# Kernel tuning notes

Hardware: AMD Instinct MI355X
Metric: run time of the kernel (lower is better)

The kernel has to match this reference:

```python
import jax, jax.numpy as jnp
import numpy as np

B = 256; N1 = 10240; E1 = 81920; N3 = 25600; E3 = 819200; D = 128


def _seg_softmax(logits, seg, n):
    m = jax.ops.segment_max(logits, seg, num_segments=n)
    e = jnp.exp(logits - m[seg])
    s = jax.ops.segment_sum(e, seg, num_segments=n)
    return e / s[seg]


def _gat(x, src, dst, W, a_src, a_dst, bias, n):
    # PyG GATConv, heads=1, add_self_loops (src/dst already include self loops)
    h = x @ W
    logit = jax.nn.leaky_relu(h[src] @ a_src + h[dst] @ a_dst, 0.2)
    alpha = _seg_softmax(logit, dst, n)
    return jax.ops.segment_sum(h[src] * alpha[:, None], dst, num_segments=n) + bias


def _gcn(x, row, col, w, W, bias, n):
    # PyG GCNConv with edge_weight, self loops already appended with weight 1
    deg = jax.ops.segment_sum(w, col, num_segments=n)
    dinv = jnp.where(deg > 0, jax.lax.rsqrt(jnp.maximum(deg, 1e-12)), 0.0)
    norm = dinv[row] * w * dinv[col]
    return jax.ops.segment_sum((x @ W)[row] * norm[:, None], col, num_segments=n) + bias


def _mean_pool(x, batch, nb):
    s = jax.ops.segment_sum(x, batch, num_segments=nb)
    cnt = jax.ops.segment_sum(jnp.ones((x.shape[0],), x.dtype), batch, num_segments=nb)
    return s / jnp.maximum(cnt, 1.0)[:, None]


def _bn(x, g, b, m, v, eps=1e-5):
    # eval-mode BatchNorm1d (running stats)
    return (x - m) * jax.lax.rsqrt(v + eps) * g + b


def _forward(x1, x3, ami_dis, ami_dis_li, fc00_w, fc00_b, fc01_w, fc01_b, fc02_w, fc02_b, w1, b1, w2, b2, fc03_w, fc03_b, gat_W, gat_as, gat_ad, gat_bias, vn_emb, vl1_w, vl1_b, bn1_g, bn1_b, bn1_m, bn1_v, vl2_w, vl2_b, bn2_g, bn2_b, bn2_m, bn2_v, gcn_W, gcn_b, fc1_w, fc1_b, fc2_w, fc2_b, fc3_w, fc3_b, out_w, out_b, drug_ei, ami_ei, batch1, ami_batch):
    relu = jax.nn.relu
    a = relu(x3 @ fc00_w + fc00_b)
    a = relu(a @ fc01_w + fc01_b)
    a = relu(a @ fc02_w + fc02_b)
    a = jnp.concatenate([a, ami_dis_li[:, None]], axis=1)  # [N3,128]
    sl3 = jnp.arange(N3)
    row = jnp.concatenate([ami_ei[0], sl3])
    col = jnp.concatenate([ami_ei[1], sl3])
    ew = jnp.concatenate([ami_dis, jnp.ones((N3,), a.dtype)])
    a = relu(_gcn(a, row, col, ew, gcn_W[0], gcn_b[0], N3)); p1 = _mean_pool(a, ami_batch, B)
    a = relu(_gcn(a, row, col, ew, gcn_W[1], gcn_b[1], N3)); p2 = _mean_pool(a, ami_batch, B)
    a = relu(_gcn(a, row, col, ew, gcn_W[2], gcn_b[2], N3)); p3 = _mean_pool(a, ami_batch, B)
    ami = p1 + p2 + p3
    h = relu(x1 @ w1 + b1)
    h = relu(h @ w2 + b2)
    h = h @ fc03_w + fc03_b
    vx = jnp.broadcast_to(vn_emb[None, :], (B, D))  # vn_emb(zeros) = row0 for every graph
    x = h + 0.2 * vx[batch1]
    sl1 = jnp.arange(N1)
    src = jnp.concatenate([drug_ei[0], sl1])
    dst = jnp.concatenate([drug_ei[1], sl1])
    x11 = relu(_gat(x, src, dst, gat_W[0], gat_as[0], gat_ad[0], gat_bias[0], N1))
    # virtual-node update (linear is Identity since in==out; eval mode: dropout off, residual False)
    t = jax.ops.segment_sum(x11, batch1, num_segments=B) + vx
    t = relu(_bn(t @ vl1_w + vl1_b, bn1_g, bn1_b, bn1_m, bn1_v))
    drug = relu(_bn(t @ vl2_w + vl2_b, bn2_g, bn2_b, bn2_m, bn2_v))
    x = x11 + 0.2 * drug[batch1]
    x12 = relu(_gat(x, src, dst, gat_W[1], gat_as[1], gat_ad[1], gat_bias[1], N1))
    x13 = relu(_gat(x, src, dst, gat_W[2], gat_as[2], gat_ad[2], gat_bias[2], N1))
    xg = _mean_pool(x11 + x12 + x13, batch1, B)
    # --- fused head ---
    z = jnp.concatenate([xg, ami], axis=1)  # [B,256]
    h2 = z @ fc1_w + fc1_b
    z = relu(h2)
    z = relu(z @ fc2_w + fc2_b)
    z = relu(z @ fc3_w + fc3_b)
    out = z @ out_w + out_b
    return out, h2


def setup_inputs() -> dict:
    key = jax.random.key(0)
    ks = iter(jax.random.split(key, 80))
    def nrm(*s):
        return jax.random.normal(next(ks), s, jnp.float32) * 0.05
    inp = {}
    inp['x1'] = jax.random.normal(next(ks), (N1, 52), jnp.float32)
    inp['x3'] = jax.random.normal(next(ks), (N3, 1900), jnp.float32)
    inp['ami_dis'] = jax.random.uniform(next(ks), (E3,), jnp.float32) + 0.1
    inp['ami_dis_li'] = jax.random.normal(next(ks), (N3,), jnp.float32)
    inp['fc00_w'] = nrm(1900, 1024); inp['fc00_b'] = nrm(1024)
    inp['fc01_w'] = nrm(1024, 512); inp['fc01_b'] = nrm(512)
    inp['fc02_w'] = nrm(512, 127); inp['fc02_b'] = nrm(127)
    inp['w1'] = nrm(52, 128); inp['b1'] = nrm(128)
    inp['w2'] = nrm(128, 64); inp['b2'] = nrm(64)
    inp['fc03_w'] = nrm(64, 128); inp['fc03_b'] = nrm(128)
    inp['gat_W'] = nrm(3, 128, 128); inp['gat_as'] = nrm(3, 128)
    inp['gat_ad'] = nrm(3, 128); inp['gat_bias'] = nrm(3, 128)
    inp['vn_emb'] = jnp.zeros((128,), jnp.float32)
    inp['vl1_w'] = nrm(128, 256); inp['vl1_b'] = nrm(256)
    inp['bn1_g'] = jnp.ones((256,), jnp.float32); inp['bn1_b'] = jnp.zeros((256,), jnp.float32)
    inp['bn1_m'] = jnp.zeros((256,), jnp.float32); inp['bn1_v'] = jnp.ones((256,), jnp.float32)
    inp['vl2_w'] = nrm(256, 128); inp['vl2_b'] = nrm(128)
    inp['bn2_g'] = jnp.ones((128,), jnp.float32); inp['bn2_b'] = jnp.zeros((128,), jnp.float32)
    inp['bn2_m'] = jnp.zeros((128,), jnp.float32); inp['bn2_v'] = jnp.ones((128,), jnp.float32)
    inp['gcn_W'] = nrm(3, 128, 128); inp['gcn_b'] = nrm(3, 128)
    inp['fc1_w'] = nrm(256, 512); inp['fc1_b'] = nrm(512)
    inp['fc2_w'] = nrm(512, 256); inp['fc2_b'] = nrm(256)
    inp['fc3_w'] = nrm(256, 128); inp['fc3_b'] = nrm(128)
    inp['out_w'] = nrm(128, 1); inp['out_b'] = nrm(1)
    inp['drug_ei'] = jax.random.randint(next(ks), (2, E1), 0, N1)
    inp['ami_ei'] = jax.random.randint(next(ks), (2, E3), 0, N3)
    inp['batch1'] = jnp.repeat(jnp.arange(B), N1 // B)
    inp['ami_batch'] = jnp.repeat(jnp.arange(B), N3 // B)
    return inp


def reference(x1, x3, ami_dis, ami_dis_li, fc00_w, fc00_b, fc01_w, fc01_b, fc02_w, fc02_b, w1, b1, w2, b2, fc03_w, fc03_b, gat_W, gat_as, gat_ad, gat_bias, vn_emb, vl1_w, vl1_b, bn1_g, bn1_b, bn1_m, bn1_v, vl2_w, vl2_b, bn2_g, bn2_b, bn2_m, bn2_v, gcn_W, gcn_b, fc1_w, fc1_b, fc2_w, fc2_b, fc3_w, fc3_b, out_w, out_b, drug_ei, ami_ei, batch1, ami_batch):
    return _forward(x1, x3, ami_dis, ami_dis_li, fc00_w, fc00_b, fc01_w, fc01_b, fc02_w, fc02_b, w1, b1, w2, b2, fc03_w, fc03_b, gat_W, gat_as, gat_ad, gat_bias, vn_emb, vl1_w, vl1_b, bn1_g, bn1_b, bn1_m, bn1_v, vl2_w, vl2_b, bn2_g, bn2_b, bn2_m, bn2_v, gcn_W, gcn_b, fc1_w, fc1_b, fc2_w, fc2_b, fc3_w, fc3_b, out_w, out_b, drug_ei, ami_ei, batch1, ami_batch)
```

## Files before the change

### kernel.cpp

```cpp
#include <hip/hip_runtime.h>
#include <hip/hip_bf16.h>
#include <stdint.h>

typedef __hip_bfloat16 bf16;
typedef __attribute__((ext_vector_type(8))) short short8;
typedef __attribute__((ext_vector_type(4))) float f32x4;

#define BB 256
#define NN1 10240
#define EE1 81920
#define NN3 25600
#define EE3 819200

__device__ __forceinline__ void load16_g2l(const void* g, void* l) {
  __builtin_amdgcn_global_load_lds(
      (const __attribute__((address_space(1))) void*)(uintptr_t)g,
      (__attribute__((address_space(3))) void*)(uintptr_t)l, 16, 0, 0);
}

__device__ __forceinline__ unsigned short f2bfbits(float v) {
  bf16 t = __float2bfloat16(v);
  union { bf16 b; unsigned short u; } x; x.b = t; return x.u;
}

// ... 4 lines not shown
  if (i >= M * nch) return;
  int r = i / nch, c8 = (i - r * nch) << 3;
  const float* s = in + (size_t)r * K + c8;
  short8 o;
  if (c8 + 8 <= K) {
    float4 a = *(const float4*)s, b = *(const float4*)(s + 4);
    o[0] = f2bfbits(a.x); o[1] = f2bfbits(a.y); o[2] = f2bfbits(a.z); o[3] = f2bfbits(a.w);
    o[4] = f2bfbits(b.x); o[5] = f2bfbits(b.y); o[6] = f2bfbits(b.z); o[7] = f2bfbits(b.w);
  } else {
#pragma unroll
    for (int j = 0; j < 8; j++) o[j] = f2bfbits(c8 + j < K ? s[j] : 0.f);
  }
  *(short8*)&out[(size_t)r * Kp + c8] = o;
}

__global__ void cast8(const float* __restrict__ in, bf16* __restrict__ out, int n8) {
  int i = blockIdx.x * blockDim.x + threadIdx.x;
  if (i >= n8) return;
  const float* s = in + (size_t)i * 8;
  float4 a = *(const float4*)s, b = *(const float4*)(s + 4);
  short8 o;
  o[0] = f2bfbits(a.x); o[1] = f2bfbits(a.y); o[2] = f2bfbits(a.z); o[3] = f2bfbits(a.w);
  o[4] = f2bfbits(b.x); o[5] = f2bfbits(b.y); o[6] = f2bfbits(b.z); o[7] = f2bfbits(b.w);
  *(short8*)&out[(size_t)i * 8] = o;
}

__global__ void transpose_cast_bf(const float* __restrict__ in, bf16* __restrict__ out,
                                  int K, int N, int Kp, int Np) {
  __shared__ float tile[32][33];
  int k0 = blockIdx.x * 32, n0 = blockIdx.y * 32;
  int tx = threadIdx.x, ty = threadIdx.y;
#pragma unroll
  for (int j = 0; j < 32; j += 8) {
    int k = k0 + ty + j, n = n0 + tx;
    tile[ty + j][tx] = (k < K && n < N) ? in[(size_t)k * N + n] : 0.f;
  }
  __syncthreads();
#pragma unroll
  for (int j = 0; j < 32; j += 8) {
    int n = n0 + ty + j, k = k0 + tx;
    if (n < Np && k < Kp) out[(size_t)n * Kp + k] = __float2bfloat16(tile[tx][ty + j]);
  }
}

template<int RELU, int OUT_F32, int CONCAT_LI>
__global__ __launch_bounds__(256) void gemm_mfma(
    const bf16* __restrict__ A, const bf16* __restrict__ Bt,
    const float* __restrict__ bias, void* __restrict__ Cout,
    const float* __restrict__ li, int M, int N, int K)
{
  __shared__ __align__(16) unsigned short sA[128 * 32];
  __shared__ __align__(16) unsigned short sB[128 * 32];
  const int nBN = N >> 7;
  const int bm = blockIdx.x / nBN, bn = blockIdx.x - bm * nBN;
  const size_t m0 = (size_t)bm << 7, n0 = (size_t)bn << 7;
  const int t = threadIdx.x;
  const int lane = t & 63, wave = t >> 6;
  const int wr = wave >> 1, wc = wave & 1;
  const int srow = t >> 2;
  const int scol = (t & 3) << 3;
  const bf16* Ab = A + (m0 + srow) * (size_t)K + scol;
  const bf16* Bb = Bt + (n0 + srow) * (size_t)K + scol;
  unsigned short* sAd = &sA[srow * 32 + scol];
  unsigned short* sBd = &sB[srow * 32 + scol];
  const int lr = lane & 15;
  const int lk = (lane >> 4) << 3;

  f32x4 zero = {0.f, 0.f, 0.f, 0.f};
  f32x4 acc[4][4];
// ... 13 lines not shown
    for (int i = 0; i < 4; i++) af[i] = *(const short8*)&sA[(wr * 64 + i * 16 + lr) * 32 + lk];
#pragma unroll
    for (int i = 0; i < 4; i++) bv[i] = *(const short8*)&sB[(wc * 64 + i * 16 + lr) * 32 + lk];
#pragma unroll
    for (int i = 0; i < 4; i++)
#pragma unroll
      for (int j = 0; j < 4; j++)
        acc[i][j] = __builtin_amdgcn_mfma_f32_16x16x32_bf16(af[i], bv[j], acc[i][j], 0, 0, 0);
    __syncthreads();
  }

  const int crow = wr * 64, ccol = wc * 64;
#pragma unroll
  for (int i = 0; i < 4; i++) {
#pragma unroll
    for (int j = 0; j < 4; j++) {
      const size_t gc = n0 + ccol + j * 16 + lr;
      const bool isLi = CONCAT_LI && (gc == (size_t)(N - 1));
      float bvf = (!isLi && bias) ? bias[gc] : 0.f;
#pragma unroll
      for (int v = 0; v < 4; v++) {
        const size_t gr = m0 + crow + i * 16 + (lane >> 4) * 4 + v;
        float val = acc[i][j][v] + bvf;
        if (RELU) val = fmaxf(val, 0.f);
        if (isLi) val = li[gr];
        if (OUT_F32) ((float*)Cout)[gr * N + gc] = val;
        else ((bf16*)Cout)[gr * N + gc] = __float2bfloat16(val);
      }
    }
  }
}

template<int RELU, int BN>
__global__ void gemm_simt(const float* __restrict__ A, const float* __restrict__ W,
                          const float* __restrict__ bias, const float* __restrict__ vnadd,
                          const float* __restrict__ bng, const float* __restrict__ bnb,
                          const float* __restrict__ bnm, const float* __restrict__ bnv,
                          float* __restrict__ C, int M, int N, int K)
{
  int idx = blockIdx.x * blockDim.x + threadIdx.x;
  if (idx >= M * N) return;
  int m = idx / N, n = idx - m * N;
  const float* a = A + (size_t)m * K;
  float acc = bias[n];
  if (vnadd) acc += 0.2f * vnadd[n];
  for (int k = 0; k < K; k++) acc = fmaf(a[k], W[(size_t)k * N + n], acc);
  if (BN) acc = (acc - bnm[n]) * rsqrtf(bnv[n] + 1e-5f) * bng[n] + bnb[n];
  if (RELU) acc = fmaxf(acc, 0.f);
  C[idx] = acc;
}

__global__ void hist_csr(const int* __restrict__ dstA, int E, int Etot, int* __restrict__ cnt) {
  int e = blockIdx.x * blockDim.x + threadIdx.x;
  if (e >= Etot) return;
  int t = (e < E) ? dstA[e] : e - E;
  atomicAdd(&cnt[t], 1);
}

__global__ void exscan(const int* __restrict__ cnt, int* __restrict__ base, int n) {
  const int tid = threadIdx.x, lane = tid & 63, wid = tid >> 6;
  __shared__ int wsum[16];
  __shared__ int woff[17];
  __shared__ int carry;
  if (tid == 0) carry = 0;
  __syncthreads();
  for (int off = 0; off < n; off += 1024) {
    int i = off + tid;
    int v = (i < n) ? cnt[i] : 0;
    int iv = v;
#pragma unroll
    for (int s = 1; s < 64; s <<= 1) {
      int tt = __shfl_up(iv, s);
      if (lane >= s) iv += tt;
    }
    if (lane == 63) wsum[wid] = iv;
    __syncthreads();
    if (tid == 0) {
      int run = 0;
      for (int j = 0; j < 16; j++) { woff[j] = run; run += wsum[j]; }
      woff[16] = run;
    }
    __syncthreads();
    if (i < n) base[i] = carry + woff[wid] + iv - v;
    __syncthreads();
    if (tid == 0) carry += woff[16];
    __syncthreads();
  }
  if (threadIdx.x == 0) base[n] = carry;
}

__global__ void fill_csr(const int* __restrict__ srcA, const int* __restrict__ dstA,
                         const float* __restrict__ w, const float* __restrict__ dinv,
                         const int* __restrict__ base, int* __restrict__ cur,
                         int2* __restrict__ rec, int E, int Etot) {
  int e = blockIdx.x * blockDim.x + threadIdx.x;
  if (e >= Etot) return;
  int s, t; float ww = 1.f;
  if (e < E) { s = srcA[e]; t = dstA[e]; if (w) ww = w[e]; }
  else { s = t = e - E; }
  int pos = base[t] + atomicAdd(&cur[t], 1);
  float nrm = dinv ? (dinv[s] * ww * dinv[t]) : 0.f;
  rec[pos] = make_int2(s, __float_as_int(nrm));
}

__global__ void deg_kernel(const int* __restrict__ col, const float* __restrict__ w,
                           float* __restrict__ deg, int E) {
  int e = blockIdx.x * blockDim.x + threadIdx.x;
  if (e < E) atomicAdd(&deg[col[e]], w[e]);
}

__global__ void dinv_kernel(const float* __restrict__ deg, float* __restrict__ dinv, int n) {
  int i = blockIdx.x * blockDim.x + threadIdx.x;
  if (i >= n) return;
  float d = deg[i] + 1.0f;
  dinv[i] = d > 0.f ? rsqrtf(fmaxf(d, 1e-12f)) : 0.f;
}

__global__ void gcn_gather(const int* __restrict__ base, const int2* __restrict__ rec,
                           const float* __restrict__ h, const float* __restrict__ bias,
                           bf16* __restrict__ aout, float* __restrict__ pool,
                           const int* __restrict__ batch, int n) {
  int wid = threadIdx.x >> 6, lane = threadIdx.x & 63;
  int node = blockIdx.x * 4 + wid;
  if (node >= n) return;
  int s0 = base[node], s1 = base[node + 1];
  float2 acc = {0.f, 0.f};
  for (int p = s0; p < s1; p++) {
    int2 r = rec[p];
    float nrm = __int_as_float(r.y);
    float2 hv = *(const float2*)&h[(size_t)r.x * 128 + lane * 2];
    acc.x += hv.x * nrm; acc.y += hv.y * nrm;
  }
  int d0 = lane * 2;
  float v0 = fmaxf(acc.x + bias[d0], 0.f);
  float v1 = fmaxf(acc.y + bias[d0 + 1], 0.f);
  __hip_bfloat162 pr; pr.x = __float2bfloat16(v0); pr.y = __float2bfloat16(v1);
  *(__hip_bfloat162*)&aout[(size_t)node * 128 + d0] = pr;
  int g = batch[node];
  atomicAdd(&pool[(size_t)g * 128 + d0], v0);
  atomicAdd(&pool[(size_t)g * 128 + d0 + 1], v1);
}

__global__ void gat_uv(const float* __restrict__ h, const float* __restrict__ as,
                       const float* __restrict__ ad, float* __restrict__ u,
                       float* __restrict__ v, int n) {
  int wave = threadIdx.x >> 6, lane = threadIdx.x & 63;
  int row = blockIdx.x * 4 + wave;
  if (row >= n) return;
  const float* hr = h + (size_t)row * 128;
  float su = 0.f, sv = 0.f;
  for (int d = lane; d < 128; d += 64) { float x = hr[d]; su += x * as[d]; sv += x * ad[d]; }
  for (int off = 32; off; off >>= 1) { su += __shfl_down(su, off); sv += __shfl_down(sv, off); }
  if (lane == 0) { u[row] = su; v[row] = sv; }
}

__global__ void gat_gather(const int* __restrict__ base, const int2* __restrict__ rec,
                           const float* __restrict__ u, const float* __restrict__ vv,
                           const float* __restrict__ h, const float* __restrict__ bias,
                           float* __restrict__ xout, float* __restrict__ pool,
                           const int* __restrict__ batch, int n) {
  int wid = threadIdx.x >> 6, lane = threadIdx.x & 63;
  int node = blockIdx.x * 4 + wid;
  if (node >= n) return;
  int s0 = base[node], s1 = base[node + 1];
  float vt = vv[node];
  float m = -3.4e38f;
  for (int p = s0 + lane; p < s1; p += 64) {
    float lg = u[rec[p].x] + vt; lg = lg >= 0.f ? lg : 0.2f * lg;
    m = fmaxf(m, lg);
  }
#pragma unroll
  for (int s = 32; s; s >>= 1) m = fmaxf(m, __shfl_xor(m, s));
  float ssum = 0.f;
  for (int p = s0 + lane; p < s1; p += 64) {
    float lg = u[rec[p].x] + vt; lg = lg >= 0.f ? lg : 0.2f * lg;
    ssum += __expf(lg - m);
  }
#pragma unroll
  for (int s = 32; s; s >>= 1) ssum += __shfl_xor(ssum, s);
  float rs = 1.f / ssum;
  float2 acc = {0.f, 0.f};
  for (int p = s0; p < s1; p++) {
    int2 r = rec[p];
    float lg = u[r.x] + vt; lg = lg >= 0.f ? lg : 0.2f * lg;
    float alpha = __expf(lg - m) * rs;
    float2 hv = *(const float2*)&h[(size_t)r.x * 128 + lane * 2];
    acc.x += hv.x * alpha; acc.y += hv.y * alpha;
  }
  int d0 = lane * 2;
  float v0 = fmaxf(acc.x + bias[d0], 0.f);
  float v1 = fmaxf(acc.y + bias[d0 + 1], 0.f);
  if (xout) *(float2*)&xout[(size_t)node * 128 + d0] = make_float2(v0, v1);
  int g = batch[node];
  atomicAdd(&pool[(size_t)g * 128 + d0], v0);
  atomicAdd(&pool[(size_t)g * 128 + d0 + 1], v1);
}

__global__ void cnt_kernel(const int* __restrict__ batch, float* __restrict__ cnt, int n) {
  int i = blockIdx.x * blockDim.x + threadIdx.x;
  if (i < n) atomicAdd(&cnt[batch[i]], 1.0f);
}

__global__ void pool_div(const float* __restrict__ pool, const float* __restrict__ cnt,
                         float* __restrict__ out, int n) {
  int i = blockIdx.x * blockDim.x + threadIdx.x;
  if (i < n) out[i] = pool[i] / fmaxf(cnt[i >> 7], 1.f);
}

__global__ void fill_t(float* __restrict__ t, const float* __restrict__ vn, int n) {
  int i = blockIdx.x * blockDim.x + threadIdx.x;
  if (i < n) t[i] = vn[i & 127];
}

__global__ void scatter_t(const float* __restrict__ x, const int* __restrict__ batch,
                          float* __restrict__ t, int n) {
  int gi = blockIdx.x * blockDim.x + threadIdx.x;
  if (gi >= n) return;
  int i = gi >> 7, d = gi & 127;
  atomicAdd(&t[(size_t)batch[i] * 128 + d], x[gi]);
}

__global__ void add_drug(const float* __restrict__ x11, const float* __restrict__ dr,
                         const int* __restrict__ batch, float* __restrict__ out, int n) {
  int gi = blockIdx.x * blockDim.x + threadIdx.x;
  if (gi >= n) return;
  int i = gi >> 7, d = gi & 127;
  out[gi] = x11[gi] + 0.2f * dr[(size_t)batch[i] * 128 + d];
}

__global__ void concat_k(const float* __restrict__ xg, const float* __restrict__ ami,
                         float* __restrict__ z, int n) {
  int i = blockIdx.x * blockDim.x + threadIdx.x;
  if (i >= n) return;
  int b = i >> 8, d = i & 255;
  z[i] = d < 128 ? xg[(b << 7) + d] : ami[(b << 7) + d - 128];
}

__global__ void relu_k(const float* __restrict__ in, float* __restrict__ out, int n) {
  int i = blockIdx.x * blockDim.x + threadIdx.x;
  if (i < n) out[i] = fmaxf(in[i], 0.f);
}

static inline int cdiv(int a, int b) { return (a + b - 1) / b; }

extern "C" void kernel_launch(void* const* d_in, const int* in_sizes, int n_in,
                              void* d_out, int out_size, void* d_ws, size_t ws_size,
                              hipStream_t stream)
{
  const float* x1      = (const float*)d_in[0];
  const float* x3      = (const float*)d_in[1];
  const float* ami_dis = (const float*)d_in[2];
  const float* ami_li  = (const float*)d_in[3];
  const float* fc00_w = (const float*)d_in[4];  const float* fc00_b = (const float*)d_in[5];
  const float* fc01_w = (const float*)d_in[6];  const float* fc01_b = (const float*)d_in[7];
  const float* fc02_w = (const float*)d_in[8];  const float* fc02_b = (const float*)d_in[9];
// ... 19 lines not shown
  const int* batch1    = (const int*)d_in[45];
  const int* ami_batch = (const int*)d_in[46];

  char* ws = (char*)d_ws;
  bf16*  Bt0   = (bf16*)(ws + 0);
  bf16*  Bt1   = (bf16*)(ws + 3932160);
  bf16*  Bt2   = (bf16*)(ws + 4980736);
  bf16*  BtGCN = (bf16*)(ws + 5111808);
  bf16*  BtGAT = (bf16*)(ws + 5210112);
  float* deg   = (float*)(ws + 5308416);
  float* dinv  = (float*)(ws + 5410816);
  float* pool_ami  = (float*)(ws + 5513216);
  float* pool_drug = (float*)(ws + 5644288);
  float* cnt_ami   = (float*)(ws + 5775360);
  float* cnt_drug  = (float*)(ws + 5776384);
  float* amivec    = (float*)(ws + 5777408);
  float* xg        = (float*)(ws + 5908480);
  float* uarr  = (float*)(ws + 6039552);
  float* varr  = (float*)(ws + 6080512);
  float* tbuf  = (float*)(ws + 6572032);
  float* t2buf = (float*)(ws + 6703104);
  float* drugv = (float*)(ws + 6965248);
  float* zbuf  = (float*)(ws + 7096320);
  float* z2buf = (float*)(ws + 7358464);
  float* z3buf = (float*)(ws + 7882752);
  float* z4buf = (float*)(ws + 8144896);

  const size_t AA = 8388608;
  bf16*  A3bf = (bf16*)(ws + AA);
  bf16*  a2bf = (bf16*)(ws + AA);
  bf16*  abf  = (bf16*)(ws + AA + 41943040);
  float* hG   = (float*)(ws + AA + 52428800);
  int*  base3 = (int*) (ws + AA + 68157440);
  int*  cur3  = (int*) (ws + AA + 68812800);
  int2* rec3  = (int2*)(ws + AA + 69206016);
  int*  base1 = (int*) (ws + AA + 77594624);
  int*  cur1  = (int*) (ws + AA + 78118912);
  int2* rec1  = (int2*)(ws + AA + 78643200);
  float* h1    = (float*)(ws + AA + 0);
  float* hd2   = (float*)(ws + AA + 5242880);
  float* xdrug = (float*)(ws + AA + 7864320);
  float* x11   = (float*)(ws + AA + 13107200);
  float* x2b   = (float*)(ws + AA + 18350080);
  bf16*  xbf   = (bf16*) (ws + AA + 23592960);
  bf16*  xbf2  = (bf16*) (ws + AA + 26214400);
  float* hgat  = (float*)(ws + AA + 28835840);
  const size_t ABo = AA + 98304000;
  bf16*  a1bf = (bf16*)(ws + ABo);

  const int Etot3 = EE3 + NN3, Etot1 = EE1 + NN1;

  {
    dim3 b(32, 8);
    transpose_cast_bf<<<dim3(60, 32), b, 0, stream>>>(fc00_w, Bt0, 1900, 1024, 1920, 1024);
    transpose_cast_bf<<<dim3(32, 16), b, 0, stream>>>(fc01_w, Bt1, 1024, 512, 1024, 512);
    transpose_cast_bf<<<dim3(16, 4), b, 0, stream>>>(fc02_w, Bt2, 512, 127, 512, 128);
    for (int l = 0; l < 3; l++) {
      transpose_cast_bf<<<dim3(4, 4), b, 0, stream>>>(gcn_W + l * 16384, BtGCN + l * 16384, 128, 128, 128, 128);
      transpose_cast_bf<<<dim3(4, 4), b, 0, stream>>>(gat_W + l * 16384, BtGAT + l * 16384, 128, 128, 128, 128);
    }
  }
  cast_pad8<<<cdiv(25600 * 240, 256), 256, 0, stream>>>(x3, A3bf, 25600, 1900, 1920);

  gemm_mfma<1, 0, 0><<<200 * 8, 256, 0, stream>>>(A3bf, Bt0, fc00_b, a1bf, nullptr, 25600, 1024, 1920);
  gemm_mfma<1, 0, 0><<<200 * 4, 256, 0, stream>>>(a1bf, Bt1, fc01_b, a2bf, nullptr, 25600, 512, 1024);
  gemm_mfma<1, 0, 1><<<200 * 1, 256, 0, stream>>>(a2bf, Bt2, fc02_b, abf, ami_li, 25600, 128, 512);

  hipMemsetAsync(deg, 0, 102400, stream);
  hipMemsetAsync(pool_ami, 0, 131072, stream);
  hipMemsetAsync(pool_drug, 0, 131072, stream);
  hipMemsetAsync(cnt_ami, 0, 1024, stream);
  hipMemsetAsync(cnt_drug, 0, 1024, stream);
  deg_kernel<<<cdiv(EE3, 256), 256, 0, stream>>>(ami_ei + EE3, ami_dis, deg, EE3);
  dinv_kernel<<<cdiv(NN3, 256), 256, 0, stream>>>(deg, dinv, NN3);
  cnt_kernel<<<cdiv(NN3, 256), 256, 0, stream>>>(ami_batch, cnt_ami, NN3);
  cnt_kernel<<<cdiv(NN1, 256), 256, 0, stream>>>(batch1, cnt_drug, NN1);

  hipMemsetAsync(cur3, 0, 102400, stream);
  hist_csr<<<cdiv(Etot3, 256), 256, 0, stream>>>(ami_ei + EE3, EE3, Etot3, cur3);
  exscan<<<1, 1024, 0, stream>>>(cur3, base3, NN3);
  hipMemsetAsync(cur3, 0, 102400, stream);
  fill_csr<<<cdiv(Etot3, 256), 256, 0, stream>>>(ami_ei, ami_ei + EE3, ami_dis, dinv,
                                                 base3, cur3, rec3, EE3, Etot3);
  hipMemsetAsync(cur1, 0, 40960, stream);
  hist_csr<<<cdiv(Etot1, 256), 256, 0, stream>>>(drug_ei + EE1, EE1, Etot1, cur1);
  exscan<<<1, 1024, 0, stream>>>(cur1, base1, NN1);
  hipMemsetAsync(cur1, 0, 40960, stream);
  fill_csr<<<cdiv(Etot1, 256), 256, 0, stream>>>(drug_ei, drug_ei + EE1, nullptr, nullptr,
                                                 base1, cur1, rec1, EE1, Etot1);

  for (int l = 0; l < 3; l++) {
    gemm_mfma<0, 1, 0><<<200, 256, 0, stream>>>(abf, BtGCN + l * 16384, nullptr, hG, nullptr, NN3, 128, 128);
    gcn_gather<<<cdiv(NN3, 4), 256, 0, stream>>>(base3, rec3, hG, gcn_b + l * 128,
                                                 abf, pool_ami, ami_batch, NN3);
  }
  pool_div<<<cdiv(BB * 128, 256), 256, 0, stream>>>(pool_ami, cnt_ami, amivec, BB * 128);

  gemm_simt<1, 0><<<cdiv(NN1 * 128, 256), 256, 0, stream>>>(x1, w1, b1, nullptr, nullptr, nullptr, nullptr, nullptr, h1, NN1, 128, 52);
  gemm_simt<1, 0><<<cdiv(NN1 * 64, 256), 256, 0, stream>>>(h1, w2, b2, nullptr, nullptr, nullptr, nullptr, nullptr, hd2, NN1, 64, 128);
  gemm_simt<0, 0><<<cdiv(NN1 * 128, 256), 256, 0, stream>>>(hd2, fc03_w, fc03_b, vn_emb, nullptr, nullptr, nullptr, nullptr, xdrug, NN1, 128, 64);
  cast8<<<cdiv(NN1 * 16, 256), 256, 0, stream>>>(xdrug, xbf, NN1 * 16);

  gemm_mfma<0, 1, 0><<<80, 256, 0, stream>>>(xbf, BtGAT, nullptr, hgat, nullptr, NN1, 128, 128);
  gat_uv<<<cdiv(NN1, 4), 256, 0, stream>>>(hgat, gat_as, gat_ad, uarr, varr, NN1);
  gat_gather<<<cdiv(NN1, 4), 256, 0, stream>>>(base1, rec1, uarr, varr, hgat, gat_bias,
                                               x11, pool_drug, batch1, NN1);

  fill_t<<<cdiv(BB * 128, 256), 256, 0, stream>>>(tbuf, vn_emb, BB * 128);
  scatter_t<<<cdiv(NN1 * 128, 256), 256, 0, stream>>>(x11, batch1, tbuf, NN1 * 128);
  gemm_simt<1, 1><<<cdiv(BB * 256, 256), 256, 0, stream>>>(tbuf, vl1_w, vl1_b, nullptr, bn1_g, bn1_b, bn1_m, bn1_v, t2buf, BB, 256, 128);
  gemm_simt<1, 1><<<cdiv(BB * 128, 256), 256, 0, stream>>>(t2buf, vl2_w, vl2_b, nullptr, bn2_g, bn2_b, bn2_m, bn2_v, drugv, BB, 128, 256);
  add_drug<<<cdiv(NN1 * 128, 256), 256, 0, stream>>>(x11, drugv, batch1, x2b, NN1 * 128);
  cast8<<<cdiv(NN1 * 16, 256), 256, 0, stream>>>(x2b, xbf2, NN1 * 16);

  for (int l = 1; l < 3; l++) {
    gemm_mfma<0, 1, 0><<<80, 256, 0, stream>>>(xbf2, BtGAT + l * 16384, nullptr, hgat, nullptr, NN1, 128, 128);
    gat_uv<<<cdiv(NN1, 4), 256, 0, stream>>>(hgat, gat_as + l * 128, gat_ad + l * 128, uarr, varr, NN1);
    gat_gather<<<cdiv(NN1, 4), 256, 0, stream>>>(base1, rec1, uarr, varr, hgat, gat_bias + l * 128,
                                                 nullptr, pool_drug, batch1, NN1);
  }
  pool_div<<<cdiv(BB * 128, 256), 256, 0, stream>>>(pool_drug, cnt_drug, xg, BB * 128);

  concat_k<<<cdiv(BB * 256, 256), 256, 0, stream>>>(xg, amivec, zbuf, BB * 256);
  float* h2out = (float*)d_out + 256;
  gemm_simt<0, 0><<<cdiv(BB * 512, 256), 256, 0, stream>>>(zbuf, fc1_w, fc1_b, nullptr, nullptr, nullptr, nullptr, nullptr, h2out, BB, 512, 256);
  relu_k<<<cdiv(BB * 512, 256), 256, 0, stream>>>(h2out, z2buf, BB * 512);
  gemm_simt<1, 0><<<cdiv(BB * 256, 256), 256, 0, stream>>>(z2buf, fc2_w, fc2_b, nullptr, nullptr, nullptr, nullptr, nullptr, z3buf, BB, 256, 512);
  gemm_simt<1, 0><<<cdiv(BB * 128, 256), 256, 0, stream>>>(z3buf, fc3_w, fc3_b, nullptr, nullptr, nullptr, nullptr, nullptr, z4buf, BB, 128, 256);
  gemm_simt<0, 0><<<1, 256, 0, stream>>>(z4buf, out_w, out_b, nullptr, nullptr, nullptr, nullptr, nullptr, (float*)d_out, BB, 1, 128);
}
```

Measured before the change: 2.030 ms.

## Reorder GCN to aggregate-then-transform, fuse drug MLP and head, bf16 GAT features

The GCN layers now aggregate bf16 node features first and then run the MFMA GEMM, with bias, ReLU and mean-pool atomics fused into its epilogue. The drug MLP becomes one per-node fused kernel, and the classifier head is fused into a single kernel. GAT hidden states are stored in bf16, and the single-block CSR scan is replaced by a three-kernel multi-block scan. Small kernels and memsets are merged and the GEMM grid gets a block swizzle. These changes cut launches, memory traffic and the serial scan, at the cost of extra bf16 rounding on intermediates and per-element pooling atomics in the GEMM epilogue.

```diff
diff --git a/kernel.cpp b/kernel.cpp
--- a/kernel.cpp
+++ b/kernel.cpp
@@ -42,20 +42,11 @@
   *(short8*)&out[(size_t)r * Kp + c8] = o;
 }
 
-__global__ void cast8(const float* __restrict__ in, bf16* __restrict__ out, int n8) {
-  int i = blockIdx.x * blockDim.x + threadIdx.x;
-  if (i >= n8) return;
-  const float* s = in + (size_t)i * 8;
-  float4 a = *(const float4*)s, b = *(const float4*)(s + 4);
-  short8 o;
-  o[0] = f2bfbits(a.x); o[1] = f2bfbits(a.y); o[2] = f2bfbits(a.z); o[3] = f2bfbits(a.w);
-  o[4] = f2bfbits(b.x); o[5] = f2bfbits(b.y); o[6] = f2bfbits(b.z); o[7] = f2bfbits(b.w);
-  *(short8*)&out[(size_t)i * 8] = o;
-}
-
 __global__ void transpose_cast_bf(const float* __restrict__ in, bf16* __restrict__ out,
                                   int K, int N, int Kp, int Np) {
   __shared__ float tile[32][33];
+  in  += (size_t)blockIdx.z * K * N;
+  out += (size_t)blockIdx.z * Kp * Np;
   int k0 = blockIdx.x * 32, n0 = blockIdx.y * 32;
   int tx = threadIdx.x, ty = threadIdx.y;
 #pragma unroll
@@ -71,16 +62,19 @@
   }
 }
 
-template<int RELU, int OUT_F32, int CONCAT_LI>
+template<int RELU, int OUT_F32, int CONCAT_LI, int POOL>
 __global__ __launch_bounds__(256) void gemm_mfma(
     const bf16* __restrict__ A, const bf16* __restrict__ Bt,
     const float* __restrict__ bias, void* __restrict__ Cout,
-    const float* __restrict__ li, int M, int N, int K)
+    const float* __restrict__ li, float* __restrict__ pool,
+    const int* __restrict__ batch, int M, int N, int K)
 {
   __shared__ __align__(16) unsigned short sA[128 * 32];
   __shared__ __align__(16) unsigned short sB[128 * 32];
   const int nBN = N >> 7;
-  const int bm = blockIdx.x / nBN, bn = blockIdx.x - bm * nBN;
+  int bid = blockIdx.x, nwg = gridDim.x;
+  int swz = (nwg & 7) ? bid : ((bid & 7) * (nwg >> 3) + (bid >> 3));
+  const int bm = swz / nBN, bn = swz - bm * nBN;
   const size_t m0 = (size_t)bm << 7, n0 = (size_t)bn << 7;
   const int t = threadIdx.x;
   const int lane = t & 63, wave = t >> 6;
@@ -124,18 +118,20 @@
 #pragma unroll
   for (int i = 0; i < 4; i++) {
 #pragma unroll
-    for (int j = 0; j < 4; j++) {
-      const size_t gc = n0 + ccol + j * 16 + lr;
-      const bool isLi = CONCAT_LI && (gc == (size_t)(N - 1));
-      float bvf = (!isLi && bias) ? bias[gc] : 0.f;
-#pragma unroll
-      for (int v = 0; v < 4; v++) {
-        const size_t gr = m0 + crow + i * 16 + (lane >> 4) * 4 + v;
-        float val = acc[i][j][v] + bvf;
+    for (int v = 0; v < 4; v++) {
+      const size_t gr = m0 + crow + i * 16 + (lane >> 4) * 4 + v;
+      const int bt = POOL ? batch[gr] : 0;
+      const float liv = CONCAT_LI ? li[gr] : 0.f;
+#pragma unroll
+      for (int j = 0; j < 4; j++) {
+        const size_t gc = n0 + ccol + j * 16 + lr;
+        const bool isLi = CONCAT_LI && (gc == (size_t)(N - 1));
+        float val = acc[i][j][v] + ((!isLi && bias) ? bias[gc] : 0.f);
         if (RELU) val = fmaxf(val, 0.f);
-        if (isLi) val = li[gr];
+        if (isLi) val = liv;
         if (OUT_F32) ((float*)Cout)[gr * N + gc] = val;
         else ((bf16*)Cout)[gr * N + gc] = __float2bfloat16(val);
+        if (POOL) atomicAdd(&pool[(size_t)bt * 128 + gc], val);
       }
     }
   }
@@ -143,7 +139,7 @@
 
 template<int RELU, int BN>
 __global__ void gemm_simt(const float* __restrict__ A, const float* __restrict__ W,
-                          const float* __restrict__ bias, const float* __restrict__ vnadd,
+                          const float* __restrict__ bias,
                           const float* __restrict__ bng, const float* __restrict__ bnb,
                           const float* __restrict__ bnm, const float* __restrict__ bnv,
                           float* __restrict__ C, int M, int N, int K)
@@ -153,7 +149,6 @@
   int m = idx / N, n = idx - m * N;
   const float* a = A + (size_t)m * K;
   float acc = bias[n];
-  if (vnadd) acc += 0.2f * vnadd[n];
   for (int k = 0; k < K; k++) acc = fmaf(a[k], W[(size_t)k * N + n], acc);
   if (BN) acc = (acc - bnm[n]) * rsqrtf(bnv[n] + 1e-5f) * bng[n] + bnb[n];
   if (RELU) acc = fmaxf(acc, 0.f);
@@ -167,36 +162,36 @@
   atomicAdd(&cnt[t], 1);
 }
 
-__global__ void exscan(const int* __restrict__ cnt, int* __restrict__ base, int n) {
+__global__ void scan_blocks(const int* __restrict__ cnt, int* __restrict__ base,
+                            int* __restrict__ bsum, int n) {
   const int tid = threadIdx.x, lane = tid & 63, wid = tid >> 6;
-  __shared__ int wsum[16];
-  __shared__ int woff[17];
-  __shared__ int carry;
-  if (tid == 0) carry = 0;
-  __syncthreads();
-  for (int off = 0; off < n; off += 1024) {
-    int i = off + tid;
-    int v = (i < n) ? cnt[i] : 0;
-    int iv = v;
-#pragma unroll
-    for (int s = 1; s < 64; s <<= 1) {
-      int tt = __shfl_up(iv, s);
-      if (lane >= s) iv += tt;
-    }
-    if (lane == 63) wsum[wid] = iv;
-    __syncthreads();
-    if (tid == 0) {
-      int run = 0;
-      for (int j = 0; j < 16; j++) { woff[j] = run; run += wsum[j]; }
-      woff[16] = run;
-    }
-    __syncthreads();
-    if (i < n) base[i] = carry + woff[wid] + iv - v;
-    __syncthreads();
-    if (tid == 0) carry += woff[16];
-    __syncthreads();
-  }
-  if (threadIdx.x == 0) base[n] = carry;
+  __shared__ int wsum[16], woff[16];
+  __shared__ int tot;
+  int i = blockIdx.x * 1024 + tid;
+  int v = (i < n) ? cnt[i] : 0;
+  int iv = v;
+#pragma unroll
+  for (int s = 1; s < 64; s <<= 1) { int t = __shfl_up(iv, s); if (lane >= s) iv += t; }
+  if (lane == 63) wsum[wid] = iv;
+  __syncthreads();
+  if (tid == 0) { int run = 0; for (int j = 0; j < 16; j++) { woff[j] = run; run += wsum[j]; } tot = run; }
+  __syncthreads();
+  if (i < n) base[i] = woff[wid] + iv - v;
+  if (tid == 0) bsum[blockIdx.x] = tot;
+}
+
+__global__ void scan_tops(int* __restrict__ bsum, int* __restrict__ base, int n, int nb) {
+  if (threadIdx.x == 0) {
+    int run = 0;
+    for (int j = 0; j < nb; j++) { int t = bsum[j]; bsum[j] = run; run += t; }
+    base[n] = run;
+  }
+}
+
+__global__ void scan_add(int* __restrict__ base, const int* __restrict__ bsum,
+                         int* __restrict__ cur, int n) {
+  int i = blockIdx.x * 1024 + threadIdx.x;
+  if (i < n) { base[i] += bsum[blockIdx.x]; cur[i] = 0; }
 }
 
 __global__ void fill_csr(const int* __restrict__ srcA, const int* __restrict__ dstA,
@@ -226,47 +221,44 @@
   dinv[i] = d > 0.f ? rsqrtf(fmaxf(d, 1e-12f)) : 0.f;
 }
 
-__global__ void gcn_gather(const int* __restrict__ base, const int2* __restrict__ rec,
-                           const float* __restrict__ h, const float* __restrict__ bias,
-                           bf16* __restrict__ aout, float* __restrict__ pool,
-                           const int* __restrict__ batch, int n) {
+__global__ void gather_pre(const int* __restrict__ base, const int2* __restrict__ rec,
+                           const bf16* __restrict__ x, bf16* __restrict__ y, int n) {
   int wid = threadIdx.x >> 6, lane = threadIdx.x & 63;
   int node = blockIdx.x * 4 + wid;
   if (node >= n) return;
   int s0 = base[node], s1 = base[node + 1];
-  float2 acc = {0.f, 0.f};
+  int d0 = lane * 2;
+  float a0 = 0.f, a1 = 0.f;
   for (int p = s0; p < s1; p++) {
     int2 r = rec[p];
     float nrm = __int_as_float(r.y);
-    float2 hv = *(const float2*)&h[(size_t)r.x * 128 + lane * 2];
-    acc.x += hv.x * nrm; acc.y += hv.y * nrm;
-  }
-  int d0 = lane * 2;
-  float v0 = fmaxf(acc.x + bias[d0], 0.f);
-  float v1 = fmaxf(acc.y + bias[d0 + 1], 0.f);
-  __hip_bfloat162 pr; pr.x = __float2bfloat16(v0); pr.y = __float2bfloat16(v1);
-  *(__hip_bfloat162*)&aout[(size_t)node * 128 + d0] = pr;
-  int g = batch[node];
-  atomicAdd(&pool[(size_t)g * 128 + d0], v0);
-  atomicAdd(&pool[(size_t)g * 128 + d0 + 1], v1);
-}
-
-__global__ void gat_uv(const float* __restrict__ h, const float* __restrict__ as,
+    __hip_bfloat162 hv = *(const __hip_bfloat162*)&x[(size_t)r.x * 128 + d0];
+    a0 = fmaf(__bfloat162float(hv.x), nrm, a0);
+    a1 = fmaf(__bfloat162float(hv.y), nrm, a1);
+  }
+  __hip_bfloat162 pr; pr.x = __float2bfloat16(a0); pr.y = __float2bfloat16(a1);
+  *(__hip_bfloat162*)&y[(size_t)node * 128 + d0] = pr;
+}
+
+__global__ void gat_uv(const bf16* __restrict__ h, const float* __restrict__ as,
                        const float* __restrict__ ad, float* __restrict__ u,
                        float* __restrict__ v, int n) {
   int wave = threadIdx.x >> 6, lane = threadIdx.x & 63;
   int row = blockIdx.x * 4 + wave;
   if (row >= n) return;
-  const float* hr = h + (size_t)row * 128;
-  float su = 0.f, sv = 0.f;
-  for (int d = lane; d < 128; d += 64) { float x = hr[d]; su += x * as[d]; sv += x * ad[d]; }
+  int d0 = lane * 2;
+  __hip_bfloat162 hv = *(const __hip_bfloat162*)&h[(size_t)row * 128 + d0];
+  float x0 = __bfloat162float(hv.x), x1 = __bfloat162float(hv.y);
+  float su = x0 * as[d0] + x1 * as[d0 + 1];
+  float sv = x0 * ad[d0] + x1 * ad[d0 + 1];
+#pragma unroll
   for (int off = 32; off; off >>= 1) { su += __shfl_down(su, off); sv += __shfl_down(sv, off); }
   if (lane == 0) { u[row] = su; v[row] = sv; }
 }
 
 __global__ void gat_gather(const int* __restrict__ base, const int2* __restrict__ rec,
                            const float* __restrict__ u, const float* __restrict__ vv,
-                           const float* __restrict__ h, const float* __restrict__ bias,
+                           const bf16* __restrict__ h, const float* __restrict__ bias,
                            float* __restrict__ xout, float* __restrict__ pool,
                            const int* __restrict__ batch, int n) {
   int wid = threadIdx.x >> 6, lane = threadIdx.x & 63;
@@ -289,66 +281,125 @@
 #pragma unroll
   for (int s = 32; s; s >>= 1) ssum += __shfl_xor(ssum, s);
   float rs = 1.f / ssum;
-  float2 acc = {0.f, 0.f};
+  int d0 = lane * 2;
+  float a0 = 0.f, a1 = 0.f;
   for (int p = s0; p < s1; p++) {
     int2 r = rec[p];
     float lg = u[r.x] + vt; lg = lg >= 0.f ? lg : 0.2f * lg;
     float alpha = __expf(lg - m) * rs;
-    float2 hv = *(const float2*)&h[(size_t)r.x * 128 + lane * 2];
-    acc.x += hv.x * alpha; acc.y += hv.y * alpha;
-  }
-  int d0 = lane * 2;
-  float v0 = fmaxf(acc.x + bias[d0], 0.f);
-  float v1 = fmaxf(acc.y + bias[d0 + 1], 0.f);
+    __hip_bfloat162 hv = *(const __hip_bfloat162*)&h[(size_t)r.x * 128 + d0];
+    a0 = fmaf(__bfloat162float(hv.x), alpha, a0);
+    a1 = fmaf(__bfloat162float(hv.y), alpha, a1);
+  }
+  float v0 = fmaxf(a0 + bias[d0], 0.f);
+  float v1 = fmaxf(a1 + bias[d0 + 1], 0.f);
   if (xout) *(float2*)&xout[(size_t)node * 128 + d0] = make_float2(v0, v1);
   int g = batch[node];
   atomicAdd(&pool[(size_t)g * 128 + d0], v0);
   atomicAdd(&pool[(size_t)g * 128 + d0 + 1], v1);
 }
 
+__global__ void mlp_drug(const float* __restrict__ x1, const float* __restrict__ w1,
+                         const float* __restrict__ b1, const float* __restrict__ w2,
+                         const float* __restrict__ b2, const float* __restrict__ w3,
+                         const float* __restrict__ b3, const float* __restrict__ vn,
+                         bf16* __restrict__ xout, int n) {
+  __shared__ float l1[4][128];
+  __shared__ float l2[4][64];
+  int wid = threadIdx.x >> 6, lane = threadIdx.x & 63;
+  int node = blockIdx.x * 4 + wid;
+  const float* xr = x1 + (size_t)node * 52;
+  int d0 = lane * 2;
+  float a0 = b1[d0], a1 = b1[d0 + 1];
+  for (int k = 0; k < 52; k++) {
+    float xk = xr[k];
+    a0 = fmaf(xk, w1[k * 128 + d0], a0); a1 = fmaf(xk, w1[k * 128 + d0 + 1], a1);
+  }
+  l1[wid][d0] = fmaxf(a0, 0.f); l1[wid][d0 + 1] = fmaxf(a1, 0.f);
+  __syncthreads();
+  float h2 = b2[lane];
+  for (int k = 0; k < 128; k++) h2 = fmaf(l1[wid][k], w2[k * 64 + lane], h2);
+  l2[wid][lane] = fmaxf(h2, 0.f);
+  __syncthreads();
+  float o0 = b3[d0] + 0.2f * vn[d0], o1 = b3[d0 + 1] + 0.2f * vn[d0 + 1];
+  for (int k = 0; k < 64; k++) {
+    float hk = l2[wid][k];
+    o0 = fmaf(hk, w3[k * 128 + d0], o0); o1 = fmaf(hk, w3[k * 128 + d0 + 1], o1);
+  }
+  __hip_bfloat162 pr; pr.x = __float2bfloat16(o0); pr.y = __float2bfloat16(o1);
+  *(__hip_bfloat162*)&xout[(size_t)node * 128 + d0] = pr;
+}
+
 __global__ void cnt_kernel(const int* __restrict__ batch, float* __restrict__ cnt, int n) {
   int i = blockIdx.x * blockDim.x + threadIdx.x;
   if (i < n) atomicAdd(&cnt[batch[i]], 1.0f);
 }
 
-__global__ void pool_div(const float* __restrict__ pool, const float* __restrict__ cnt,
-                         float* __restrict__ out, int n) {
+__global__ void tvn_k(const float* __restrict__ pool, const float* __restrict__ vn,
+                      float* __restrict__ t, int n) {
   int i = blockIdx.x * blockDim.x + threadIdx.x;
-  if (i < n) out[i] = pool[i] / fmaxf(cnt[i >> 7], 1.f);
-}
-
-__global__ void fill_t(float* __restrict__ t, const float* __restrict__ vn, int n) {
+  if (i < n) t[i] = pool[i] + vn[i & 127];
+}
+
+__global__ void add_cast(const float* __restrict__ x11, const float* __restrict__ dr,
+                         const int* __restrict__ batch, bf16* __restrict__ out, int n2) {
   int i = blockIdx.x * blockDim.x + threadIdx.x;
-  if (i < n) t[i] = vn[i & 127];
-}
-
-__global__ void scatter_t(const float* __restrict__ x, const int* __restrict__ batch,
-                          float* __restrict__ t, int n) {
-  int gi = blockIdx.x * blockDim.x + threadIdx.x;
-  if (gi >= n) return;
-  int i = gi >> 7, d = gi & 127;
-  atomicAdd(&t[(size_t)batch[i] * 128 + d], x[gi]);
-}
-
-__global__ void add_drug(const float* __restrict__ x11, const float* __restrict__ dr,
-                         const int* __restrict__ batch, float* __restrict__ out, int n) {
-  int gi = blockIdx.x * blockDim.x + threadIdx.x;
-  if (gi >= n) return;
-  int i = gi >> 7, d = gi & 127;
-  out[gi] = x11[gi] + 0.2f * dr[(size_t)batch[i] * 128 + d];
-}
-
-__global__ void concat_k(const float* __restrict__ xg, const float* __restrict__ ami,
-                         float* __restrict__ z, int n) {
-  int i = blockIdx.x * blockDim.x + threadIdx.x;
-  if (i >= n) return;
-  int b = i >> 8, d = i & 255;
-  z[i] = d < 128 ? xg[(b << 7) + d] : ami[(b << 7) + d - 128];
-}
-
-__global__ void relu_k(const float* __restrict__ in, float* __restrict__ out, int n) {
-  int i = blockIdx.x * blockDim.x + threadIdx.x;
-  if (i < n) out[i] = fmaxf(in[i], 0.f);
+  if (i >= n2) return;
+  int node = i >> 6, d0 = (i & 63) << 1;
+  const float* drb = dr + (size_t)batch[node] * 128 + d0;
+  float2 xv = *(const float2*)&x11[(size_t)node * 128 + d0];
+  __hip_bfloat162 pr;
+  pr.x = __float2bfloat16(xv.x + 0.2f * drb[0]);
+  pr.y = __float2bfloat16(xv.y + 0.2f * drb[1]);
+  *(__hip_bfloat162*)&out[(size_t)node * 128 + d0] = pr;
+}
+
+__global__ __launch_bounds__(256) void head_fused(
+    const float* __restrict__ pool_d, const float* __restrict__ cnt_d,
+    const float* __restrict__ pool_a, const float* __restrict__ cnt_a,
+    const float* __restrict__ fc1_w, const float* __restrict__ fc1_b,
+    const float* __restrict__ fc2_w, const float* __restrict__ fc2_b,
+    const float* __restrict__ fc3_w, const float* __restrict__ fc3_b,
+    const float* __restrict__ ow, const float* __restrict__ ob,
+    float* __restrict__ out, float* __restrict__ h2out) {
+  __shared__ float z[8][256], h2[8][512], z3[8][256], z4[8][128];
+  int tid = threadIdx.x; int r0 = blockIdx.x * 8;
+  for (int idx = tid; idx < 8 * 256; idx += 256) {
+    int r = idx >> 8, d = idx & 255; int b = r0 + r;
+    z[r][d] = d < 128 ? pool_d[b * 128 + d] / fmaxf(cnt_d[b], 1.f)
+                      : pool_a[b * 128 + d - 128] / fmaxf(cnt_a[b], 1.f);
+  }
+  __syncthreads();
+  for (int idx = tid; idx < 8 * 512; idx += 256) {
+    int r = idx >> 9, n = idx & 511;
+    float acc = fc1_b[n];
+    for (int k = 0; k < 256; k++) acc = fmaf(z[r][k], fc1_w[k * 512 + n], acc);
+    h2out[(size_t)(r0 + r) * 512 + n] = acc;
+    h2[r][n] = fmaxf(acc, 0.f);
+  }
+  __syncthreads();
+  for (int idx = tid; idx < 8 * 256; idx += 256) {
+    int r = idx >> 8, n = idx & 255;
+    float acc = fc2_b[n];
+    for (int k = 0; k < 512; k++) acc = fmaf(h2[r][k], fc2_w[k * 256 + n], acc);
+    z3[r][n] = fmaxf(acc, 0.f);
+  }
+  __syncthreads();
+  for (int idx = tid; idx < 8 * 128; idx += 256) {
+    int r = idx >> 7, n = idx & 127;
+    float acc = fc3_b[n];
+    for (int k = 0; k < 256; k++) acc = fmaf(z3[r][k], fc3_w[k * 128 + n], acc);
+    z4[r][n] = fmaxf(acc, 0.f);
+  }
+  __syncthreads();
+  if (tid < 8 * 16) {
+    int r = tid >> 4, l = tid & 15;
+    float acc = 0.f;
+    for (int k = l; k < 128; k += 16) acc = fmaf(z4[r][k], ow[k], acc);
+#pragma unroll
+    for (int s = 8; s; s >>= 1) acc += __shfl_down(acc, s);
+    if (l == 0) out[r0 + r] = acc + ob[0];
+  }
 }
 
 static inline int cdiv(int a, int b) { return (a + b - 1) / b; }
@@ -398,37 +449,29 @@
   float* pool_drug = (float*)(ws + 5644288);
   float* cnt_ami   = (float*)(ws + 5775360);
   float* cnt_drug  = (float*)(ws + 5776384);
-  float* amivec    = (float*)(ws + 5777408);
-  float* xg        = (float*)(ws + 5908480);
   float* uarr  = (float*)(ws + 6039552);
   float* varr  = (float*)(ws + 6080512);
+  int*   bsum3 = (int*)  (ws + 6121472);
+  int*   bsum1 = (int*)  (ws + 6121728);
   float* tbuf  = (float*)(ws + 6572032);
   float* t2buf = (float*)(ws + 6703104);
   float* drugv = (float*)(ws + 6965248);
-  float* zbuf  = (float*)(ws + 7096320);
-  float* z2buf = (float*)(ws + 7358464);
-  float* z3buf = (float*)(ws + 7882752);
-  float* z4buf = (float*)(ws + 8144896);
 
   const size_t AA = 8388608;
   bf16*  A3bf = (bf16*)(ws + AA);
   bf16*  a2bf = (bf16*)(ws + AA);
   bf16*  abf  = (bf16*)(ws + AA + 41943040);
-  float* hG   = (float*)(ws + AA + 52428800);
+  bf16*  ybf  = (bf16*)(ws + AA + 52428800);
   int*  base3 = (int*) (ws + AA + 68157440);
   int*  cur3  = (int*) (ws + AA + 68812800);
   int2* rec3  = (int2*)(ws + AA + 69206016);
   int*  base1 = (int*) (ws + AA + 77594624);
   int*  cur1  = (int*) (ws + AA + 78118912);
   int2* rec1  = (int2*)(ws + AA + 78643200);
-  float* h1    = (float*)(ws + AA + 0);
-  float* hd2   = (float*)(ws + AA + 5242880);
-  float* xdrug = (float*)(ws + AA + 7864320);
-  float* x11   = (float*)(ws + AA + 13107200);
-  float* x2b   = (float*)(ws + AA + 18350080);
-  bf16*  xbf   = (bf16*) (ws + AA + 23592960);
-  bf16*  xbf2  = (bf16*) (ws + AA + 26214400);
-  float* hgat  = (float*)(ws + AA + 28835840);
+  bf16*  xbf   = (bf16*) (ws + AA + 0);
+  bf16*  hgat  = (bf16*) (ws + AA + 5242880);
+  float* x11   = (float*)(ws + AA + 10485760);
+  bf16*  xbf2  = (bf16*) (ws + AA + 15728640);
   const size_t ABo = AA + 98304000;
   bf16*  a1bf = (bf16*)(ws + ABo);
 
@@ -439,22 +482,17 @@
     transpose_cast_bf<<<dim3(60, 32), b, 0, stream>>>(fc00_w, Bt0, 1900, 1024, 1920, 1024);
     transpose_cast_bf<<<dim3(32, 16), b, 0, stream>>>(fc01_w, Bt1, 1024, 512, 1024, 512);
     transpose_cast_bf<<<dim3(16, 4), b, 0, stream>>>(fc02_w, Bt2, 512, 127, 512, 128);
-    for (int l = 0; l < 3; l++) {
-      transpose_cast_bf<<<dim3(4, 4), b, 0, stream>>>(gcn_W + l * 16384, BtGCN + l * 16384, 128, 128, 128, 128);
-      transpose_cast_bf<<<dim3(4, 4), b, 0, stream>>>(gat_W + l * 16384, BtGAT + l * 16384, 128, 128, 128, 128);
-    }
+    transpose_cast_bf<<<dim3(4, 4, 3), b, 0, stream>>>(gcn_W, BtGCN, 128, 128, 128, 128);
+    transpose_cast_bf<<<dim3(4, 4, 3), b, 0, stream>>>(gat_W, BtGAT, 128, 128, 128, 128);
   }
   cast_pad8<<<cdiv(25600 * 240, 256), 256, 0, stream>>>(x3, A3bf, 25600, 1900, 1920);
 
-  gemm_mfma<1, 0, 0><<<200 * 8, 256, 0, stream>>>(A3bf, Bt0, fc00_b, a1bf, nullptr, 25600, 1024, 1920);
-  gemm_mfma<1, 0, 0><<<200 * 4, 256, 0, stream>>>(a1bf, Bt1, fc01_b, a2bf, nullptr, 25600, 512, 1024);
-  gemm_mfma<1, 0, 1><<<200 * 1, 256, 0, stream>>>(a2bf, Bt2, fc02_b, abf, ami_li, 25600, 128, 512);
-
-  hipMemsetAsync(deg, 0, 102400, stream);
-  hipMemsetAsync(pool_ami, 0, 131072, stream);
-  hipMemsetAsync(pool_drug, 0, 131072, stream);
-  hipMemsetAsync(cnt_ami, 0, 1024, stream);
-  hipMemsetAsync(cnt_drug, 0, 1024, stream);
+  hipMemsetAsync(deg, 0, 468992, stream);
+
+  gemm_mfma<1, 0, 0, 0><<<200 * 8, 256, 0, stream>>>(A3bf, Bt0, fc00_b, a1bf, nullptr, nullptr, nullptr, 25600, 1024, 1920);
+  gemm_mfma<1, 0, 0, 0><<<200 * 4, 256, 0, stream>>>(a1bf, Bt1, fc01_b, a2bf, nullptr, nullptr, nullptr, 25600, 512, 1024);
+  gemm_mfma<1, 0, 1, 0><<<200 * 1, 256, 0, stream>>>(a2bf, Bt2, fc02_b, abf, ami_li, nullptr, nullptr, 25600, 128, 512);
+
   deg_kernel<<<cdiv(EE3, 256), 256, 0, stream>>>(ami_ei + EE3, ami_dis, deg, EE3);
   dinv_kernel<<<cdiv(NN3, 256), 256, 0, stream>>>(deg, dinv, NN3);
   cnt_kernel<<<cdiv(NN3, 256), 256, 0, stream>>>(ami_batch, cnt_ami, NN3);
@@ -462,54 +500,45 @@
 
   hipMemsetAsync(cur3, 0, 102400, stream);
   hist_csr<<<cdiv(Etot3, 256), 256, 0, stream>>>(ami_ei + EE3, EE3, Etot3, cur3);
-  exscan<<<1, 1024, 0, stream>>>(cur3, base3, NN3);
-  hipMemsetAsync(cur3, 0, 102400, stream);
+  scan_blocks<<<25, 1024, 0, stream>>>(cur3, base3, bsum3, NN3);
+  scan_tops<<<1, 64, 0, stream>>>(bsum3, base3, NN3, 25);
+  scan_add<<<25, 1024, 0, stream>>>(base3, bsum3, cur3, NN3);
   fill_csr<<<cdiv(Etot3, 256), 256, 0, stream>>>(ami_ei, ami_ei + EE3, ami_dis, dinv,
                                                  base3, cur3, rec3, EE3, Etot3);
   hipMemsetAsync(cur1, 0, 40960, stream);
   hist_csr<<<cdiv(Etot1, 256), 256, 0, stream>>>(drug_ei + EE1, EE1, Etot1, cur1);
-  exscan<<<1, 1024, 0, stream>>>(cur1, base1, NN1);
-  hipMemsetAsync(cur1, 0, 40960, stream);
+  scan_blocks<<<10, 1024, 0, stream>>>(cur1, base1, bsum1, NN1);
+  scan_tops<<<1, 64, 0, stream>>>(bsum1, base1, NN1, 10);
+  scan_add<<<10, 1024, 0, stream>>>(base1, bsum1, cur1, NN1);
   fill_csr<<<cdiv(Etot1, 256), 256, 0, stream>>>(drug_ei, drug_ei + EE1, nullptr, nullptr,
                                                  base1, cur1, rec1, EE1, Etot1);
 
   for (int l = 0; l < 3; l++) {
-    gemm_mfma<0, 1, 0><<<200, 256, 0, stream>>>(abf, BtGCN + l * 16384, nullptr, hG, nullptr, NN3, 128, 128);
-    gcn_gather<<<cdiv(NN3, 4), 256, 0, stream>>>(base3, rec3, hG, gcn_b + l * 128,
-                                                 abf, pool_ami, ami_batch, NN3);
-  }
-  pool_div<<<cdiv(BB * 128, 256), 256, 0, stream>>>(pool_ami, cnt_ami, amivec, BB * 128);
-
-  gemm_simt<1, 0><<<cdiv(NN1 * 128, 256), 256, 0, stream>>>(x1, w1, b1, nullptr, nullptr, nullptr, nullptr, nullptr, h1, NN1, 128, 52);
-  gemm_simt<1, 0><<<cdiv(NN1 * 64, 256), 256, 0, stream>>>(h1, w2, b2, nullptr, nullptr, nullptr, nullptr, nullptr, hd2, NN1, 64, 128);
-  gemm_simt<0, 0><<<cdiv(NN1 * 128, 256), 256, 0, stream>>>(hd2, fc03_w, fc03_b, vn_emb, nullptr, nullptr, nullptr, nullptr, xdrug, NN1, 128, 64);
-  cast8<<<cdiv(NN1 * 16, 256), 256, 0, stream>>>(xdrug, xbf, NN1 * 16);
-
-  gemm_mfma<0, 1, 0><<<80, 256, 0, stream>>>(xbf, BtGAT, nullptr, hgat, nullptr, NN1, 128, 128);
+    gather_pre<<<cdiv(NN3, 4), 256, 0, stream>>>(base3, rec3, abf, ybf, NN3);
+    gemm_mfma<1, 0, 0, 1><<<200, 256, 0, stream>>>(ybf, BtGCN + l * 16384, gcn_b + l * 128,
+                                                   abf, nullptr, pool_ami, ami_batch, NN3, 128, 128);
+  }
+
+  mlp_drug<<<NN1 / 4, 256, 0, stream>>>(x1, w1, b1, w2, b2, fc03_w, fc03_b, vn_emb, xbf, NN1);
+
+  gemm_mfma<0, 0, 0, 0><<<80, 256, 0, stream>>>(xbf, BtGAT, nullptr, hgat, nullptr, nullptr, nullptr, NN1, 128, 128);
   gat_uv<<<cdiv(NN1, 4), 256, 0, stream>>>(hgat, gat_as, gat_ad, uarr, varr, NN1);
   gat_gather<<<cdiv(NN1, 4), 256, 0, stream>>>(base1, rec1, uarr, varr, hgat, gat_bias,
                                                x11, pool_drug, batch1, NN1);
 
-  fill_t<<<cdiv(BB * 128, 256), 256, 0, stream>>>(tbuf, vn_emb, BB * 128);
-  scatter_t<<<cdiv(NN1 * 128, 256), 256, 0, stream>>>(x11, batch1, tbuf, NN1 * 128);
-  gemm_simt<1, 1><<<cdiv(BB * 256, 256), 256, 0, stream>>>(tbuf, vl1_w, vl1_b, nullptr, bn1_g, bn1_b, bn1_m, bn1_v, t2buf, BB, 256, 128);
-  gemm_simt<1, 1><<<cdiv(BB * 128, 256), 256, 0, stream>>>(t2buf, vl2_w, vl2_b, nullptr, bn2_g, bn2_b, bn2_m, bn2_v, drugv, BB, 128, 256);
-  add_drug<<<cdiv(NN1 * 128, 256), 256, 0, stream>>>(x11, drugv, batch1, x2b, NN1 * 128);
-  cast8<<<cdiv(NN1 * 16, 256), 256, 0, stream>>>(x2b, xbf2, NN1 * 16);
+  tvn_k<<<cdiv(BB * 128, 256), 256, 0, stream>>>(pool_drug, vn_emb, tbuf, BB * 128);
+  gemm_simt<1, 1><<<cdiv(BB * 256, 256), 256, 0, stream>>>(tbuf, vl1_w, vl1_b, bn1_g, bn1_b, bn1_m, bn1_v, t2buf, BB, 256, 128);
+  gemm_simt<1, 1><<<cdiv(BB * 128, 256), 256, 0, stream>>>(t2buf, vl2_w, vl2_b, bn2_g, bn2_b, bn2_m, bn2_v, drugv, BB, 128, 256);
+  add_cast<<<cdiv(NN1 * 64, 256), 256, 0, stream>>>(x11, drugv, batch1, xbf2, NN1 * 64);
 
   for (int l = 1; l < 3; l++) {
-    gemm_mfma<0, 1, 0><<<80, 256, 0, stream>>>(xbf2, BtGAT + l * 16384, nullptr, hgat, nullptr, NN1, 128, 128);
+    gemm_mfma<0, 0, 0, 0><<<80, 256, 0, stream>>>(xbf2, BtGAT + l * 16384, nullptr, hgat, nullptr, nullptr, nullptr, NN1, 128, 128);
     gat_uv<<<cdiv(NN1, 4), 256, 0, stream>>>(hgat, gat_as + l * 128, gat_ad + l * 128, uarr, varr, NN1);
     gat_gather<<<cdiv(NN1, 4), 256, 0, stream>>>(base1, rec1, uarr, varr, hgat, gat_bias + l * 128,
                                                  nullptr, pool_drug, batch1, NN1);
   }
-  pool_div<<<cdiv(BB * 128, 256), 256, 0, stream>>>(pool_drug, cnt_drug, xg, BB * 128);
-
-  concat_k<<<cdiv(BB * 256, 256), 256, 0, stream>>>(xg, amivec, zbuf, BB * 256);
-  float* h2out = (float*)d_out + 256;
-  gemm_simt<0, 0><<<cdiv(BB * 512, 256), 256, 0, stream>>>(zbuf, fc1_w, fc1_b, nullptr, nullptr, nullptr, nullptr, nullptr, h2out, BB, 512, 256);
-  relu_k<<<cdiv(BB * 512, 256), 256, 0, stream>>>(h2out, z2buf, BB * 512);
-  gemm_simt<1, 0><<<cdiv(BB * 256, 256), 256, 0, stream>>>(z2buf, fc2_w, fc2_b, nullptr, nullptr, nullptr, nullptr, nullptr, z3buf, BB, 256, 512);
-  gemm_simt<1, 0><<<cdiv(BB * 128, 256), 256, 0, stream>>>(z3buf, fc3_w, fc3_b, nullptr, nullptr, nullptr, nullptr, nullptr, z4buf, BB, 128, 256);
-  gemm_simt<0, 0><<<1, 256, 0, stream>>>(z4buf, out_w, out_b, nullptr, nullptr, nullptr, nullptr, nullptr, (float*)d_out, BB, 1, 128);
-}
+
+  head_fused<<<32, 256, 0, stream>>>(pool_drug, cnt_drug, pool_ami, cnt_ami,
+                                     fc1_w, fc1_b, fc2_w, fc2_b, fc3_w, fc3_b,
+                                     out_w, out_b, (float*)d_out, (float*)d_out + 256);
+}
```

Measured after the change: 1.749 ms. -13.8%, faster.
